# Performance work log

Hardware: AMD Instinct MI355X
Metric: run time of the kernel (lower is better)

Reference implementation:

```python
import jax, jax.numpy as jnp
import numpy as np

SPARSITY = 0.5  # cur_sparsity set during training; 0.0 default would make masking a no-op
WEIGHT_BETA = 1.0
MASK_ALPHA1 = 1.0
MASK_ALPHA2 = 1.0


def binarize(mask_scores, sparsity):
    # SparseBinarizer.forward: prune (set to 0) the `num_prune` smallest scores globally.
    num_prune = int(mask_scores.size * sparsity)  # static: sparsity is a Python float
    flat = mask_scores.reshape(-1)
    prune_idx = jnp.argsort(flat)[:num_prune]
    mask = jnp.ones_like(flat).at[prune_idx].set(0.0)
    return mask.reshape(mask_scores.shape)


def setup_inputs() -> dict:
    key = jax.random.key(0)
    ks = jax.random.split(key, 9)
    out_f, in_f, r = 4096, 4096, 8
    tokens = 8192  # batch 4 * seq 2048
    return {
        "x": jax.random.normal(ks[0], (tokens, in_f), dtype=jnp.float32),
        "weight": jax.random.normal(ks[1], (out_f, in_f), dtype=jnp.float32) * 0.02,
        "bias": jax.random.normal(ks[2], (out_f,), dtype=jnp.float32) * 0.02,
        "weight_U": jax.random.normal(ks[3], (out_f, r), dtype=jnp.float32),
        "weight_V": jnp.zeros((r, in_f), dtype=jnp.float32),
        "mask_scores_A": jax.random.normal(ks[4], (out_f, r), dtype=jnp.float32),
        "mask_scores_B": jnp.zeros((r, in_f), dtype=jnp.float32),
        "mask_scores_R": jnp.zeros((out_f,), dtype=jnp.float32),
        "mask_scores_C": jnp.zeros((in_f,), dtype=jnp.float32),
    }


def reference(x, weight, bias, weight_U, weight_V, mask_scores_A, mask_scores_B,
              mask_scores_R, mask_scores_C):
    # weight = W + beta * U @ V   (low-rank weight reconstruction)
    w = weight + WEIGHT_BETA * (weight_U @ weight_V)
    # mask_scores = |w| + a1 * A @ B + a2 * (R[:,None] + C[None,:])
    mask_scores = (jnp.abs(w)
                   + MASK_ALPHA1 * (mask_scores_A @ mask_scores_B)
                   + MASK_ALPHA2 * (mask_scores_R[:, None] + mask_scores_C[None, :]))
    mask = binarize(mask_scores, SPARSITY)
    masked_weight = mask * w  # [out_f, in_f]
    # nn.Linear: x @ W^T + b
    return x @ masked_weight.T + bias
```

## Files before the change

### kernel.cpp

```cpp
#include <hip/hip_runtime.h>
#include <stdint.h>

#define TOKENS 8192
#define OUT_F  4096
#define IN_F   4096
#define RNK    8
#define RPB    4
#define KPRUNE 8388608u
#define TIECAP 4096u

typedef unsigned short u16;
typedef float  f32x4  __attribute__((ext_vector_type(4)));
typedef short  bf16x8 __attribute__((ext_vector_type(8)));
typedef unsigned short u16x8 __attribute__((ext_vector_type(8)));

#define XB_OFF    0ull
#define WB_OFF    67108864ull
#define KEYS_OFF  100663296ull
#define CTL_OFF   167772160ull
#define H1_OFF    0
#define H2_OFF    16384
#define H3_OFF    32768
#define SEL_OFF   33792
#define TIECNT_OFF 33824
#define TIEIDX_OFF 33828
#define CTL_ZERO_U32 8457

__device__ __forceinline__ u16 f2bf(float f) {
    uint32_t u = __float_as_uint(f);
    u += 0x7fffu + ((u >> 16) & 1u);
    return (u16)(u >> 16);
}

__device__ __forceinline__ uint32_t fkey(float s) {
    uint32_t u = __float_as_uint(s);
    return (u & 0x80000000u) ? ~u : (u | 0x80000000u);
}

__global__ void convx_kernel(const float* __restrict__ x, u16* __restrict__ xB,
                             uint32_t* __restrict__ ctl)
{
    const int t = threadIdx.x;
    if (blockIdx.x < 34) {
        const int i = blockIdx.x * 256 + t;
        if (i < CTL_ZERO_U32) ctl[i] = 0u;
    }
    const size_t idx = (size_t)blockIdx.x * 256 + t;
    const float4* xv = (const float4*)x;
    float4 a = xv[idx*2];
    float4 b = xv[idx*2 + 1];
    u16x8 o;
    o[0]=f2bf(a.x); o[1]=f2bf(a.y); o[2]=f2bf(a.z); o[3]=f2bf(a.w);
    o[4]=f2bf(b.x); o[5]=f2bf(b.y); o[6]=f2bf(b.z); o[7]=f2bf(b.w);
    *((u16x8*)xB + idx) = o;
}

__global__ void prep_kernel(const float* __restrict__ W, const float* __restrict__ U,
                            const float* __restrict__ V, const float* __restrict__ A,
                            const float* __restrict__ B, const float* __restrict__ R,
                            const float* __restrict__ C, u16* __restrict__ wB,
                            uint32_t* __restrict__ keys, uint32_t* __restrict__ hist1)
{
    __shared__ uint32_t lh[4096];
    const int o0 = blockIdx.x * RPB, t = threadIdx.x;
    for (int b = t; b < 4096; b += 256) lh[b] = 0u;
    float uu[RPB][RNK], aa[RPB][RNK], ro[RPB];
#pragma unroll
    for (int r0 = 0; r0 < RPB; ++r0) {
#pragma unroll
        for (int r = 0; r < RNK; ++r) {
            uu[r0][r] = U[(o0+r0)*RNK + r];
            aa[r0][r] = A[(o0+r0)*RNK + r];
        }
        ro[r0] = R[o0 + r0];
    }
    __syncthreads();
    for (int j = 0; j < IN_F/256; ++j) {
        const int i = j*256 + t;
        float vv[RNK], bb[RNK];
#pragma unroll
        for (int r = 0; r < RNK; ++r) { vv[r] = V[r*IN_F + i]; bb[r] = B[r*IN_F + i]; }
        const float ci = C[i];
#pragma unroll
        for (int r0 = 0; r0 < RPB; ++r0) {
            float wv = W[(size_t)(o0+r0)*IN_F + i];
#pragma unroll
            for (int r = 0; r < RNK; ++r) wv = fmaf(uu[r0][r], vv[r], wv);
            float s = fabsf(wv);
#pragma unroll
            for (int r = 0; r < RNK; ++r) s = fmaf(aa[r0][r], bb[r], s);
            s += ro[r0] + ci;
            const uint32_t key = fkey(s);
            keys[(size_t)(o0+r0)*IN_F + i] = key;
            wB[(size_t)(o0+r0)*IN_F + i]   = f2bf(wv);
            atomicAdd(&lh[key >> 20], 1u);
        }
    }
    __syncthreads();
    for (int b = t; b < 4096; b += 256) { uint32_t c = lh[b]; if (c) atomicAdd(&hist1[b], c); }
}

__global__ void select_kernel(const uint32_t* __restrict__ hist, uint32_t* sel, int nbins, int mode)
{
    __shared__ uint32_t lh[4096];
    __shared__ uint32_t part[256];
    __shared__ uint32_t sseg[2];
    const int t = threadIdx.x;
    const uint32_t b1v = sel[0], c1v = sel[1], b2v = sel[2], c3v = sel[3];
    uint32_t k;
    if (mode == 0)      k = KPRUNE;
    else if (mode == 1) k = KPRUNE - c1v;
    else                k = KPRUNE - c3v;
    for (int b = t; b < nbins; b += 256) lh[b] = hist[b];
    __syncthreads();
    const int per = nbins >> 8;
    uint32_t s = 0;
    for (int j = 0; j < per; ++j) s += lh[t*per + j];
    part[t] = s;
    __syncthreads();
    uint32_t pre = 0;
    for (int tt = 0; tt < t; ++tt) pre += part[tt];
    if (pre < k && pre + part[t] >= k) { sseg[0] = (uint32_t)t; sseg[1] = pre; }
    __syncthreads();
    const int seg = (int)sseg[0];
    const uint32_t accb = sseg[1];
    if (t < per) {
        uint32_t pre2 = 0;
        for (int j = 0; j < t; ++j) pre2 += lh[seg*per + j];
        const uint32_t c = lh[seg*per + t];
        const uint32_t below = accb + pre2;
        if (below < k && below + c >= k) {
            const uint32_t bin = (uint32_t)(seg*per + t);
            if (mode == 0)      { sel[0] = bin; sel[1] = below; }
            else if (mode == 1) { sel[2] = bin; sel[3] = c1v + below; }
            else {
                sel[4] = (b1v << 20) | (b2v << 8) | bin;
                sel[5] = k - below;
            }
        }
    }
}

__global__ void hist2_kernel(const uint32_t* __restrict__ keys, const uint32_t* __restrict__ sel,
                             uint32_t* __restrict__ hist2)
{
    __shared__ uint32_t lh[4096];
    const int o = blockIdx.x, t = threadIdx.x;
    const uint32_t b1 = sel[0];
    for (int b = t; b < 4096; b += 256) lh[b] = 0u;
    __syncthreads();
    const uint32_t* kp = keys + (size_t)o*IN_F + t*16;
#pragma unroll
    for (int q = 0; q < 4; ++q) {
        uint4 kv = *(const uint4*)(kp + q*4);
        if ((kv.x >> 20) == b1) atomicAdd(&lh[(kv.x >> 8) & 0xFFFu], 1u);
        if ((kv.y >> 20) == b1) atomicAdd(&lh[(kv.y >> 8) & 0xFFFu], 1u);
        if ((kv.z >> 20) == b1) atomicAdd(&lh[(kv.z >> 8) & 0xFFFu], 1u);
        if ((kv.w >> 20) == b1) atomicAdd(&lh[(kv.w >> 8) & 0xFFFu], 1u);
    }
    __syncthreads();
    for (int b = t; b < 4096; b += 256) { uint32_t c = lh[b]; if (c) atomicAdd(&hist2[b], c); }
}

__global__ void hist3_kernel(const uint32_t* __restrict__ keys, const uint32_t* __restrict__ sel,
                             uint32_t* __restrict__ hist3)
{
    __shared__ uint32_t lh[256];
    const int o = blockIdx.x, t = threadIdx.x;
    const uint32_t pfx = (sel[0] << 12) | sel[2];
    lh[t] = 0u;
    __syncthreads();
    const uint32_t* kp = keys + (size_t)o*IN_F + t*16;
#pragma unroll
    for (int q = 0; q < 4; ++q) {
        uint4 kv = *(const uint4*)(kp + q*4);
        if ((kv.x >> 8) == pfx) atomicAdd(&lh[kv.x & 0xFFu], 1u);
        if ((kv.y >> 8) == pfx) atomicAdd(&lh[kv.y & 0xFFu], 1u);
        if ((kv.z >> 8) == pfx) atomicAdd(&lh[kv.z & 0xFFu], 1u);
        if ((kv.w >> 8) == pfx) atomicAdd(&lh[kv.w & 0xFFu], 1u);
    }
    __syncthreads();
    uint32_t c = lh[t];
    if (c) atomicAdd(&hist3[t], c);
}

__global__ void apply_kernel(const uint32_t* __restrict__ keys, const uint32_t* __restrict__ sel,
                             u16* __restrict__ wB, uint32_t* __restrict__ tiecnt,
                             uint32_t* __restrict__ tieidx)
{
    const uint32_t thr = sel[4];
    const size_t base = ((size_t)blockIdx.x * 256 + threadIdx.x) * 16;
    uint32_t kv[16];
#pragma unroll
    for (int q = 0; q < 4; ++q) *(uint4*)(kv + q*4) = *(const uint4*)(keys + base + q*4);
    uint4 wraw[2];
    wraw[0] = *(const uint4*)(wB + base);
    wraw[1] = *(const uint4*)(wB + base + 8);
    u16* wv = (u16*)wraw;
#pragma unroll
    for (int e = 0; e < 16; ++e) {
        if (kv[e] < thr) wv[e] = 0u;
        else if (kv[e] == thr) {
            uint32_t slot = atomicAdd(tiecnt, 1u);
            if (slot < TIECAP) tieidx[slot] = (uint32_t)(base + e);
        }
    }
    *(uint4*)(wB + base)     = wraw[0];
    *(uint4*)(wB + base + 8) = wraw[1];
}

__global__ void fixties_kernel(const uint32_t* __restrict__ sel, const uint32_t* __restrict__ tiecnt,
                               const uint32_t* __restrict__ tieidx, u16* __restrict__ wB)
{
    const uint32_t p = sel[5];
    uint32_t n = *tiecnt; if (n > TIECAP) n = TIECAP;
    for (uint32_t i = threadIdx.x; i < n; i += 256) {
        const uint32_t my = tieidx[i];
        uint32_t rank = 0;
        for (uint32_t j = 0; j < n; ++j) rank += (tieidx[j] < my) ? 1u : 0u;
        if (rank < p) wB[my] = 0u;
    }
}

#define LA0 0
#define LB0 32768
#define LA1 65536
#define LB1 98304

__device__ __forceinline__ void gl_lds16(const char* src, char* dst) {
    __builtin_amdgcn_global_load_lds((const __attribute__((address_space(1))) void*)src,
                                     (__attribute__((address_space(3))) void*)dst, 16, 0, 0);
}

__global__ __launch_bounds__(512, 2) void gemm256_kernel(const u16* __restrict__ xB,
                                                         const u16* __restrict__ wB,
                                                         const float* __restrict__ bias,
                                                         float* __restrict__ out)
{
    __shared__ char ldsc[131072];
    const int t    = threadIdx.x;
    const int lane = t & 63;
    const int wid  = t >> 6;
    const int wm   = wid >> 2;
    const int wn   = wid & 3;
    const int bm   = blockIdx.x >> 4;
    const int bn   = blockIdx.x & 15;

    const int l15 = lane & 15;
    const int kb  = (lane >> 4) << 4;
    const int sw  = (lane & 7) << 4;
    const int bA  = (16*wm + l15) * 128 + kb;
    const int bB  = (64*wn + l15) * 128 + kb;

    const int scol = ((t & 7) * 16) ^ (((t >> 3) & 7) << 4);
    const char* pA = (const char*)xB + ((size_t)(bm*256 + (t >> 3))) * (IN_F*2) + scol;
    const char* pB = (const char*)wB + ((size_t)(bn*256 + (t >> 3))) * (IN_F*2) + scol;
    const int tb16 = t * 16;

#define STAGE(pG, reg, h, tile) do {                                          \
    const char* _s = (pG) + (size_t)(tile)*128 + (size_t)(h)*(128*IN_F*2);    \
    char* _d = ldsc + (reg) + (h)*16384 + tb16;                               \
    gl_lds16(_s, _d);                                                         \
    gl_lds16(_s + (size_t)(64*IN_F*2), _d + 8192);                            \
} while (0)

    f32x4  acc[8][4] = {};
    bf16x8 b[4][2];
    bf16x8 a[2][2];

#define LOADB(reg) do {                                                       \
    _Pragma("unroll") for (int ni = 0; ni < 4; ++ni)                          \
    _Pragma("unroll") for (int kk = 0; kk < 2; ++kk)                          \
        b[ni][kk] = *(const bf16x8*)(ldsc + (reg) +                           \
                      ((bB + ni*2048 + kk*64) ^ sw));                         \
} while (0)

#define LOADA(reg, q) do {                                                    \
    _Pragma("unroll") for (int mm = 0; mm < 2; ++mm)                          \
    _Pragma("unroll") for (int kk = 0; kk < 2; ++kk)                          \
        a[mm][kk] = *(const bf16x8*)(ldsc + (reg) +                           \
                      ((bA + (2*(q)+mm)*4096 + kk*64) ^ sw));                 \
} while (0)

#define MFMAQ(q) do {                                                         \
    _Pragma("unroll") for (int mm = 0; mm < 2; ++mm)                          \
    _Pragma("unroll") for (int ni = 0; ni < 4; ++ni)                          \
    _Pragma("unroll") for (int kk = 0; kk < 2; ++kk)                          \
        acc[2*(q)+mm][ni] = __builtin_amdgcn_mfma_f32_16x16x32_bf16(          \
            a[mm][kk], b[ni][kk], acc[2*(q)+mm][ni], 0, 0, 0);                \
} while (0)

#define PH_TAIL(q)                                                            \
    __builtin_amdgcn_s_barrier();                                             \
    asm volatile("s_waitcnt lgkmcnt(0)" ::: "memory");                        \
    __builtin_amdgcn_s_setprio(1);                                            \
    MFMAQ(q);                                                                 \
    __builtin_amdgcn_s_setprio(0);                                            \
    __builtin_amdgcn_s_barrier();

    STAGE(pB, LB0, 0, 0);
    STAGE(pB, LB0, 1, 0);
    STAGE(pA, LA0, 0, 0);
    STAGE(pA, LA0, 1, 0);
    STAGE(pB, LB1, 0, 1);
    STAGE(pB, LB1, 1, 1);
    STAGE(pA, LA1, 0, 1);
    asm volatile("s_waitcnt vmcnt(6)" ::: "memory");
    __builtin_amdgcn_s_barrier();

#pragma unroll 1
    for (int j = 0; j < IN_F/64/2; ++j) {
        const int to = 2*j + 1;
        const int se = (2*j + 2) & 63;
        const int so = (2*j + 3) & 63;

        LOADB(LB0); LOADA(LA0, 0);
        STAGE(pA, LA1, 1, to);
        asm volatile("s_waitcnt lgkmcnt(8)" ::: "memory");
        PH_TAIL(0)
        LOADA(LA0, 1);
        STAGE(pB, LB0, 0, se);
        PH_TAIL(1)
        LOADA(LA0, 2);
        STAGE(pB, LB0, 1, se);
        PH_TAIL(2)
        LOADA(LA0, 3);
        STAGE(pA, LA0, 0, se);
        asm volatile("s_waitcnt vmcnt(6)" ::: "memory");
        PH_TAIL(3)

        LOADB(LB1); LOADA(LA1, 0);
        STAGE(pA, LA0, 1, se);
        asm volatile("s_waitcnt lgkmcnt(8)" ::: "memory");
        PH_TAIL(0)
        LOADA(LA1, 1);
        STAGE(pB, LB1, 0, so);
        PH_TAIL(1)
        LOADA(LA1, 2);
        STAGE(pB, LB1, 1, so);
        PH_TAIL(2)
        LOADA(LA1, 3);
        STAGE(pA, LA1, 0, so);
        asm volatile("s_waitcnt vmcnt(6)" ::: "memory");
        PH_TAIL(3)
    }

    const int orow0 = bm*256 + 16*wm + ((lane >> 4) << 2);
    const int ocol0 = bn*256 + 64*wn + l15;
#pragma unroll
    for (int ni = 0; ni < 4; ++ni) {
        const int col = ocol0 + ni*16;
        const float bv = bias[col];
#pragma unroll
        for (int m = 0; m < 8; ++m) {
            const int r0 = orow0 + 32*m;
            f32x4 v = acc[m][ni];
#pragma unroll
            for (int q = 0; q < 4; ++q)
                out[(size_t)(r0 + q)*OUT_F + col] = v[q] + bv;
        }
    }
#undef STAGE
#undef LOADB
#undef LOADA
#undef MFMAQ
#undef PH_TAIL
}

extern "C" void kernel_launch(void* const* d_in, const int* in_sizes, int n_in,
                              void* d_out, int out_size, void* d_ws, size_t ws_size,
                              hipStream_t stream)
{
    const float* x    = (const float*)d_in[0];
    const float* W    = (const float*)d_in[1];
    const float* bias = (const float*)d_in[2];
    const float* U    = (const float*)d_in[3];
    const float* V    = (const float*)d_in[4];
    const float* A    = (const float*)d_in[5];
    const float* B    = (const float*)d_in[6];
    const float* R    = (const float*)d_in[7];
    const float* C    = (const float*)d_in[8];
    float* out = (float*)d_out;

    char* ws = (char*)d_ws;
    u16*      xB   = (u16*)(ws + XB_OFF);
    u16*      wB   = (u16*)(ws + WB_OFF);
    uint32_t* keys = (uint32_t*)(ws + KEYS_OFF);
    uint32_t* ctl  = (uint32_t*)(ws + CTL_OFF);
    uint32_t* h1   = (uint32_t*)((char*)ctl + H1_OFF);
    uint32_t* h2   = (uint32_t*)((char*)ctl + H2_OFF);
    uint32_t* h3   = (uint32_t*)((char*)ctl + H3_OFF);
    uint32_t* sel  = (uint32_t*)((char*)ctl + SEL_OFF);
    uint32_t* tiecnt = (uint32_t*)((char*)ctl + TIECNT_OFF);
    uint32_t* tieidx = (uint32_t*)((char*)ctl + TIEIDX_OFF);

    convx_kernel<<<TOKENS*IN_F/8/256, 256, 0, stream>>>(x, xB, ctl);
    prep_kernel<<<OUT_F/RPB, 256, 0, stream>>>(W, U, V, A, B, R, C, wB, keys, h1);
    select_kernel<<<1, 256, 0, stream>>>(h1, sel, 4096, 0);
    hist2_kernel<<<OUT_F, 256, 0, stream>>>(keys, sel, h2);
    select_kernel<<<1, 256, 0, stream>>>(h2, sel, 4096, 1);
    hist3_kernel<<<OUT_F, 256, 0, stream>>>(keys, sel, h3);
    select_kernel<<<1, 256, 0, stream>>>(h3, sel, 256, 2);
    apply_kernel<<<OUT_F, 256, 0, stream>>>(keys, sel, wB, tiecnt, tieidx);
    fixties_kernel<<<1, 256, 0, stream>>>(sel, tiecnt, tieidx, wB);
    gemm256_kernel<<<(TOKENS/256)*(OUT_F/256), 512, 0, stream>>>(xB, wB, bias, out);
}
```

Measured before the change: 434.1 us.

## Replace third histogram pass with candidate list, vectorise prep, remap GEMM tiles

The prep kernel now processes four columns per thread with float4 loads and splits its LDS histogram into two copies to reduce atomic contention. The third radix histogram pass, its select step and the separate tie-fix kernel are replaced by a collect pass. That pass appends only keys matching the 24-bit prefix to a global list, and a single block then selects the final threshold and resolves ties by index. The GEMM block index is remapped to change tile ordering for cache locality. The new path risks overflowing the list when more than CAP3 candidates share a prefix, and it relies on one global atomic counter.

New measurement: 459.1 us. +5.8%, slower.

```diff
diff --git a/kernel.cpp b/kernel.cpp
--- a/kernel.cpp
+++ b/kernel.cpp
@@ -7,11 +7,12 @@
 #define RNK    8
 #define RPB    4
 #define KPRUNE 8388608u
-#define TIECAP 4096u
+#define CAP3   16384u
 
 typedef unsigned short u16;
 typedef float  f32x4  __attribute__((ext_vector_type(4)));
 typedef short  bf16x8 __attribute__((ext_vector_type(8)));
+typedef unsigned short u16x4 __attribute__((ext_vector_type(4)));
 typedef unsigned short u16x8 __attribute__((ext_vector_type(8)));
 
 #define XB_OFF    0ull
@@ -20,11 +21,10 @@
 #define CTL_OFF   167772160ull
 #define H1_OFF    0
 #define H2_OFF    16384
-#define H3_OFF    32768
-#define SEL_OFF   33792
-#define TIECNT_OFF 33824
-#define TIEIDX_OFF 33828
-#define CTL_ZERO_U32 8457
+#define SEL_OFF   32768
+#define CNT3_OFF  32800
+#define LIST3_OFF 32804
+#define CTL_ZERO_U32 8201
 
 __device__ __forceinline__ u16 f2bf(float f) {
     uint32_t u = __float_as_uint(f);
@@ -61,9 +61,10 @@
                             const float* __restrict__ C, u16* __restrict__ wB,
                             uint32_t* __restrict__ keys, uint32_t* __restrict__ hist1)
 {
-    __shared__ uint32_t lh[4096];
+    __shared__ uint32_t lh[2][4096];
     const int o0 = blockIdx.x * RPB, t = threadIdx.x;
-    for (int b = t; b < 4096; b += 256) lh[b] = 0u;
+    uint32_t* lhs = lh[t & 1];
+    for (int b = t; b < 8192; b += 256) ((uint32_t*)lh)[b] = 0u;
     float uu[RPB][RNK], aa[RPB][RNK], ro[RPB];
 #pragma unroll
     for (int r0 = 0; r0 < RPB; ++r0) {
@@ -75,47 +76,61 @@
         ro[r0] = R[o0 + r0];
     }
     __syncthreads();
-    for (int j = 0; j < IN_F/256; ++j) {
-        const int i = j*256 + t;
-        float vv[RNK], bb[RNK];
-#pragma unroll
-        for (int r = 0; r < RNK; ++r) { vv[r] = V[r*IN_F + i]; bb[r] = B[r*IN_F + i]; }
-        const float ci = C[i];
+    for (int j = 0; j < IN_F/1024; ++j) {
+        const int i = j*1024 + t*4;
+        const float4 cc = *(const float4*)&C[i];
 #pragma unroll
         for (int r0 = 0; r0 < RPB; ++r0) {
-            float wv = W[(size_t)(o0+r0)*IN_F + i];
-#pragma unroll
-            for (int r = 0; r < RNK; ++r) wv = fmaf(uu[r0][r], vv[r], wv);
-            float s = fabsf(wv);
-#pragma unroll
-            for (int r = 0; r < RNK; ++r) s = fmaf(aa[r0][r], bb[r], s);
-            s += ro[r0] + ci;
-            const uint32_t key = fkey(s);
-            keys[(size_t)(o0+r0)*IN_F + i] = key;
-            wB[(size_t)(o0+r0)*IN_F + i]   = f2bf(wv);
-            atomicAdd(&lh[key >> 20], 1u);
+            float4 wv = *(const float4*)&W[(size_t)(o0+r0)*IN_F + i];
+#pragma unroll
+            for (int r = 0; r < RNK; ++r) {
+                const float4 v4 = *(const float4*)&V[r*IN_F + i];
+                const float u0 = uu[r0][r];
+                wv.x = fmaf(u0, v4.x, wv.x); wv.y = fmaf(u0, v4.y, wv.y);
+                wv.z = fmaf(u0, v4.z, wv.z); wv.w = fmaf(u0, v4.w, wv.w);
+            }
+            float4 s;
+            s.x = fabsf(wv.x); s.y = fabsf(wv.y); s.z = fabsf(wv.z); s.w = fabsf(wv.w);
+#pragma unroll
+            for (int r = 0; r < RNK; ++r) {
+                const float4 b4 = *(const float4*)&B[r*IN_F + i];
+                const float a0 = aa[r0][r];
+                s.x = fmaf(a0, b4.x, s.x); s.y = fmaf(a0, b4.y, s.y);
+                s.z = fmaf(a0, b4.z, s.z); s.w = fmaf(a0, b4.w, s.w);
+            }
+            const float rr = ro[r0];
+            s.x += rr + cc.x; s.y += rr + cc.y; s.z += rr + cc.z; s.w += rr + cc.w;
+            uint4 k4;
+            k4.x = fkey(s.x); k4.y = fkey(s.y); k4.z = fkey(s.z); k4.w = fkey(s.w);
+            *(uint4*)&keys[(size_t)(o0+r0)*IN_F + i] = k4;
+            u16x4 w4;
+            w4[0] = f2bf(wv.x); w4[1] = f2bf(wv.y); w4[2] = f2bf(wv.z); w4[3] = f2bf(wv.w);
+            *(u16x4*)&wB[(size_t)(o0+r0)*IN_F + i] = w4;
+            atomicAdd(&lhs[k4.x >> 20], 1u);
+            atomicAdd(&lhs[k4.y >> 20], 1u);
+            atomicAdd(&lhs[k4.z >> 20], 1u);
+            atomicAdd(&lhs[k4.w >> 20], 1u);
         }
     }
     __syncthreads();
-    for (int b = t; b < 4096; b += 256) { uint32_t c = lh[b]; if (c) atomicAdd(&hist1[b], c); }
-}
-
-__global__ void select_kernel(const uint32_t* __restrict__ hist, uint32_t* sel, int nbins, int mode)
+    for (int b = t; b < 4096; b += 256) {
+        const uint32_t c = lh[0][b] + lh[1][b];
+        if (c) atomicAdd(&hist1[b], c);
+    }
+}
+
+__global__ void select_kernel(const uint32_t* __restrict__ hist, uint32_t* sel, int mode)
 {
     __shared__ uint32_t lh[4096];
     __shared__ uint32_t part[256];
     __shared__ uint32_t sseg[2];
     const int t = threadIdx.x;
-    const uint32_t b1v = sel[0], c1v = sel[1], b2v = sel[2], c3v = sel[3];
-    uint32_t k;
-    if (mode == 0)      k = KPRUNE;
-    else if (mode == 1) k = KPRUNE - c1v;
-    else                k = KPRUNE - c3v;
-    for (int b = t; b < nbins; b += 256) lh[b] = hist[b];
-    __syncthreads();
-    const int per = nbins >> 8;
+    const uint32_t c1v = sel[1];
+    const uint32_t k = (mode == 0) ? KPRUNE : (KPRUNE - c1v);
+    for (int b = t; b < 4096; b += 256) lh[b] = hist[b];
+    __syncthreads();
     uint32_t s = 0;
-    for (int j = 0; j < per; ++j) s += lh[t*per + j];
+    for (int j = 0; j < 16; ++j) s += lh[t*16 + j];
     part[t] = s;
     __syncthreads();
     uint32_t pre = 0;
@@ -124,19 +139,15 @@
     __syncthreads();
     const int seg = (int)sseg[0];
     const uint32_t accb = sseg[1];
-    if (t < per) {
+    if (t < 16) {
         uint32_t pre2 = 0;
-        for (int j = 0; j < t; ++j) pre2 += lh[seg*per + j];
-        const uint32_t c = lh[seg*per + t];
+        for (int j = 0; j < t; ++j) pre2 += lh[seg*16 + j];
+        const uint32_t c = lh[seg*16 + t];
         const uint32_t below = accb + pre2;
         if (below < k && below + c >= k) {
-            const uint32_t bin = (uint32_t)(seg*per + t);
-            if (mode == 0)      { sel[0] = bin; sel[1] = below; }
-            else if (mode == 1) { sel[2] = bin; sel[3] = c1v + below; }
-            else {
-                sel[4] = (b1v << 20) | (b2v << 8) | bin;
-                sel[5] = k - below;
-            }
+            const uint32_t bin = (uint32_t)(seg*16 + t);
+            if (mode == 0) { sel[0] = bin; sel[1] = below; }
+            else           { sel[2] = bin; sel[3] = c1v + below; }
         }
     }
 }
@@ -162,31 +173,62 @@
     for (int b = t; b < 4096; b += 256) { uint32_t c = lh[b]; if (c) atomicAdd(&hist2[b], c); }
 }
 
-__global__ void hist3_kernel(const uint32_t* __restrict__ keys, const uint32_t* __restrict__ sel,
-                             uint32_t* __restrict__ hist3)
-{
-    __shared__ uint32_t lh[256];
-    const int o = blockIdx.x, t = threadIdx.x;
+__global__ void collect3_kernel(const uint32_t* __restrict__ keys, const uint32_t* __restrict__ sel,
+                                uint32_t* __restrict__ cnt3, uint32_t* __restrict__ list3)
+{
     const uint32_t pfx = (sel[0] << 12) | sel[2];
-    lh[t] = 0u;
-    __syncthreads();
-    const uint32_t* kp = keys + (size_t)o*IN_F + t*16;
+    const size_t base = ((size_t)blockIdx.x * 256 + threadIdx.x) * 16;
 #pragma unroll
     for (int q = 0; q < 4; ++q) {
-        uint4 kv = *(const uint4*)(kp + q*4);
-        if ((kv.x >> 8) == pfx) atomicAdd(&lh[kv.x & 0xFFu], 1u);
-        if ((kv.y >> 8) == pfx) atomicAdd(&lh[kv.y & 0xFFu], 1u);
-        if ((kv.z >> 8) == pfx) atomicAdd(&lh[kv.z & 0xFFu], 1u);
-        if ((kv.w >> 8) == pfx) atomicAdd(&lh[kv.w & 0xFFu], 1u);
-    }
-    __syncthreads();
-    uint32_t c = lh[t];
-    if (c) atomicAdd(&hist3[t], c);
+        uint4 kv = *(const uint4*)(keys + base + q*4);
+        const uint32_t i0 = (uint32_t)(base + q*4);
+        if ((kv.x >> 8) == pfx) { uint32_t s = atomicAdd(cnt3, 1u); if (s < CAP3) list3[s] = ((i0+0u) << 8) | (kv.x & 0xFFu); }
+        if ((kv.y >> 8) == pfx) { uint32_t s = atomicAdd(cnt3, 1u); if (s < CAP3) list3[s] = ((i0+1u) << 8) | (kv.y & 0xFFu); }
+        if ((kv.z >> 8) == pfx) { uint32_t s = atomicAdd(cnt3, 1u); if (s < CAP3) list3[s] = ((i0+2u) << 8) | (kv.z & 0xFFu); }
+        if ((kv.w >> 8) == pfx) { uint32_t s = atomicAdd(cnt3, 1u); if (s < CAP3) list3[s] = ((i0+3u) << 8) | (kv.w & 0xFFu); }
+    }
+}
+
+__global__ void selfix_kernel(uint32_t* sel, const uint32_t* __restrict__ cnt3,
+                              const uint32_t* __restrict__ list3, u16* __restrict__ wB)
+{
+    __shared__ uint32_t lst[CAP3];
+    __shared__ uint32_t hist[256];
+    __shared__ uint32_t sv[2];
+    const int t = threadIdx.x;
+    uint32_t n = *cnt3; if (n > CAP3) n = CAP3;
+    hist[t] = 0u;
+    __syncthreads();
+    for (uint32_t i = t; i < n; i += 256) {
+        const uint32_t e = list3[i];
+        lst[i] = e;
+        atomicAdd(&hist[e & 0xFFu], 1u);
+    }
+    __syncthreads();
+    const uint32_t k3 = KPRUNE - sel[3];
+    uint32_t pre = 0;
+    for (int b = 0; b < t; ++b) pre += hist[b];
+    if (pre < k3 && pre + hist[t] >= k3) {
+        sv[0] = (uint32_t)t;
+        sv[1] = k3 - pre;
+        sel[4] = (sel[0] << 20) | (sel[2] << 8) | (uint32_t)t;
+    }
+    __syncthreads();
+    const uint32_t b3 = sv[0], p = sv[1];
+    for (uint32_t i = t; i < n; i += 256) {
+        const uint32_t e = lst[i];
+        if ((e & 0xFFu) != b3) continue;
+        uint32_t rank = 0;
+        for (uint32_t j = 0; j < n; ++j) {
+            const uint32_t f = lst[j];
+            rank += ((f & 0xFFu) == b3 && f < e) ? 1u : 0u;
+        }
+        if (rank < p) wB[e >> 8] = 0u;
+    }
 }
 
 __global__ void apply_kernel(const uint32_t* __restrict__ keys, const uint32_t* __restrict__ sel,
-                             u16* __restrict__ wB, uint32_t* __restrict__ tiecnt,
-                             uint32_t* __restrict__ tieidx)
+                             u16* __restrict__ wB)
 {
     const uint32_t thr = sel[4];
     const size_t base = ((size_t)blockIdx.x * 256 + threadIdx.x) * 16;
@@ -198,28 +240,9 @@
     wraw[1] = *(const uint4*)(wB + base + 8);
     u16* wv = (u16*)wraw;
 #pragma unroll
-    for (int e = 0; e < 16; ++e) {
-        if (kv[e] < thr) wv[e] = 0u;
-        else if (kv[e] == thr) {
-            uint32_t slot = atomicAdd(tiecnt, 1u);
-            if (slot < TIECAP) tieidx[slot] = (uint32_t)(base + e);
-        }
-    }
+    for (int e = 0; e < 16; ++e) if (kv[e] < thr) wv[e] = 0u;
     *(uint4*)(wB + base)     = wraw[0];
     *(uint4*)(wB + base + 8) = wraw[1];
-}
-
-__global__ void fixties_kernel(const uint32_t* __restrict__ sel, const uint32_t* __restrict__ tiecnt,
-                               const uint32_t* __restrict__ tieidx, u16* __restrict__ wB)
-{
-    const uint32_t p = sel[5];
-    uint32_t n = *tiecnt; if (n > TIECAP) n = TIECAP;
-    for (uint32_t i = threadIdx.x; i < n; i += 256) {
-        const uint32_t my = tieidx[i];
-        uint32_t rank = 0;
-        for (uint32_t j = 0; j < n; ++j) rank += (tieidx[j] < my) ? 1u : 0u;
-        if (rank < p) wB[my] = 0u;
-    }
 }
 
 #define LA0 0
@@ -243,8 +266,10 @@
     const int wid  = t >> 6;
     const int wm   = wid >> 2;
     const int wn   = wid & 3;
-    const int bm   = blockIdx.x >> 4;
-    const int bn   = blockIdx.x & 15;
+    const int orig = blockIdx.x;
+    const int tid  = (orig & 7) * 64 + (orig >> 3);
+    const int bn   = tid >> 5;
+    const int bm   = tid & 31;
 
     const int l15 = lane & 15;
     const int kb  = (lane >> 4) << 4;
@@ -383,25 +408,23 @@
     float* out = (float*)d_out;
 
     char* ws = (char*)d_ws;
-    u16*      xB   = (u16*)(ws + XB_OFF);
-    u16*      wB   = (u16*)(ws + WB_OFF);
-    uint32_t* keys = (uint32_t*)(ws + KEYS_OFF);
-    uint32_t* ctl  = (uint32_t*)(ws + CTL_OFF);
-    uint32_t* h1   = (uint32_t*)((char*)ctl + H1_OFF);
-    uint32_t* h2   = (uint32_t*)((char*)ctl + H2_OFF);
-    uint32_t* h3   = (uint32_t*)((char*)ctl + H3_OFF);
-    uint32_t* sel  = (uint32_t*)((char*)ctl + SEL_OFF);
-    uint32_t* tiecnt = (uint32_t*)((char*)ctl + TIECNT_OFF);
-    uint32_t* tieidx = (uint32_t*)((char*)ctl + TIEIDX_OFF);
+    u16*      xB    = (u16*)(ws + XB_OFF);
+    u16*      wB    = (u16*)(ws + WB_OFF);
+    uint32_t* keys  = (uint32_t*)(ws + KEYS_OFF);
+    uint32_t* ctl   = (uint32_t*)(ws + CTL_OFF);
+    uint32_t* h1    = (uint32_t*)((char*)ctl + H1_OFF);
+    uint32_t* h2    = (uint32_t*)((char*)ctl + H2_OFF);
+    uint32_t* sel   = (uint32_t*)((char*)ctl + SEL_OFF);
+    uint32_t* cnt3  = (uint32_t*)((char*)ctl + CNT3_OFF);
+    uint32_t* list3 = (uint32_t*)((char*)ctl + LIST3_OFF);
 
     convx_kernel<<<TOKENS*IN_F/8/256, 256, 0, stream>>>(x, xB, ctl);
     prep_kernel<<<OUT_F/RPB, 256, 0, stream>>>(W, U, V, A, B, R, C, wB, keys, h1);
-    select_kernel<<<1, 256, 0, stream>>>(h1, sel, 4096, 0);
+    select_kernel<<<1, 256, 0, stream>>>(h1, sel, 0);
     hist2_kernel<<<OUT_F, 256, 0, stream>>>(keys, sel, h2);
-    select_kernel<<<1, 256, 0, stream>>>(h2, sel, 4096, 1);
-    hist3_kernel<<<OUT_F, 256, 0, stream>>>(keys, sel, h3);
-    select_kernel<<<1, 256, 0, stream>>>(h3, sel, 256, 2);
-    apply_kernel<<<OUT_F, 256, 0, stream>>>(keys, sel, wB, tiecnt, tieidx);
-    fixties_kernel<<<1, 256, 0, stream>>>(sel, tiecnt, tieidx, wB);
+    select_kernel<<<1, 256, 0, stream>>>(h2, sel, 1);
+    collect3_kernel<<<OUT_F, 256, 0, stream>>>(keys, sel, cnt3, list3);
+    selfix_kernel<<<1, 256, 0, stream>>>(sel, cnt3, list3, wB);
+    apply_kernel<<<OUT_F, 256, 0, stream>>>(keys, sel, wB);
     gemm256_kernel<<<(TOKENS/256)*(OUT_F/256), 512, 0, stream>>>(xB, wB, bias, out);
 }
```
